# Optimization experiments

Hardware: AMD Instinct MI355X
Metric: run time of the kernel (lower is better)

The kernel has to match this reference:

```python
import jax, jax.numpy as jnp
import numpy as np

LATENT_SHAPES = [(192, 2, 2), (48, 4, 4), (24, 8, 8), (12, 16, 16), (6, 32, 32)]
B = 4          # batch
M = 32         # num_bases
HT, WT = 32, 32  # target spatial size = spatial size of z[-1] = (H/2, W/2)
EPS = 1e-3
CT = sum(s[0] for s in LATENT_SHAPES)  # 282


def _forward_fft(zs):
    # strided zero-insertion upsample of each latent to (HT, WT), concat channels, 2D FFT
    ups = []
    for zi in zs:
        b, c, h, w = zi.shape
        rh, rw = HT // h, WT // w
        u = jnp.zeros((b, c, HT, WT), zi.dtype).at[..., ::rh, ::rw].set(zi)
        ups.append(u)
    z = jnp.concatenate(ups, axis=1)            # (B, CT, HT, WT)
    return jnp.fft.fftn(z, axes=(-2, -1))       # complex64


def _inverse_fft(v_fft):
    # inverse FFT, take real part, split channels per level, strided downsample
    v = jnp.fft.ifftn(v_fft, axes=(-2, -1)).real  # (B, M, CT, HT, WT)
    splits = np.cumsum([s[0] for s in LATENT_SHAPES])[:-1]
    parts = jnp.split(v, splits, axis=-3)
    out = []
    for vi, (c, h, w) in zip(parts, LATENT_SHAPES):
        rh, rw = HT // h, WT // w
        out.append(vi[..., ::rh, ::rw])           # (B, M, c, h, w)
    return out


def _vector_field(zs, L, lam):
    z_fft = _forward_fft(zs)
    La = (L - jnp.swapaxes(L, -1, -2)).astype(jnp.complex64)        # antisymmetric (M, CT, CT)
    lam_a = (lam - jnp.roll(jnp.flip(lam, (1, 2)), (1, 1), axis=(1, 2))) * 1j  # (M, HT, WT) imaginary
    v_fft = jnp.einsum('mcd,bchw->bmdhw', La, z_fft)                 # (B, M, CT, HT, WT) complex
    v_fft = v_fft * lam_a[None, :, None, :, :]
    return _inverse_fft(v_fft)


def _log_prob(ws, zs, L, lam):
    S_ww = sum(jnp.einsum('bchw,bchw->b', wi, wi) for wi in ws)      # (B,)
    v = _vector_field(zs, L, lam)
    S_zz = sum(jnp.einsum('bnchw,bmchw->bnm', vi, vi) for vi in v)   # (B, M, M)
    S_zw = sum(jnp.einsum('bnchw,bchw->bn', vi, wi) for vi, wi in zip(v, ws))  # (B, M)
    var = jnp.maximum(jnp.mean(jnp.diagonal(S_zz, axis1=-2, axis2=-1), -1), 1e-6)
    std = jnp.sqrt(var)
    S_zz = S_zz / var[:, None, None]
    S_zw = S_zw / std[:, None]
    I = jnp.eye(M, dtype=S_zz.dtype)
    Mm = S_zz + EPS * I
    trace = EPS * S_ww + jnp.einsum('bn,bn->b', S_zw, S_zw)
    Lh = jnp.linalg.cholesky(Mm)
    logdet = 2.0 * jnp.sum(jnp.log(jnp.diagonal(Lh, axis1=-2, axis2=-1)), -1)
    return 0.5 * (logdet - trace)


def setup_inputs() -> dict:
    key = jax.random.key(0)
    ks = jax.random.split(key, 12)
    inp = {}
    for i, (c, h, w) in enumerate(LATENT_SHAPES):
        inp[f'z{i}'] = jax.random.normal(ks[i], (B, c, h, w), jnp.float32)
        inp[f'w{i}'] = jax.random.normal(ks[5 + i], (B, c, h, w), jnp.float32)
    inp['L'] = jax.random.normal(ks[10], (M, CT, CT), jnp.float32) * np.float32(1.0 / np.sqrt(CT))
    inp['lam'] = jax.random.normal(ks[11], (M, HT, WT), jnp.float32)
    return inp


def reference(z0, z1, z2, z3, z4, w0, w1, w2, w3, w4, L, lam):
    return _log_prob([w0, w1, w2, w3, w4], [z0, z1, z2, z3, z4], L, lam)
```

## Files before the change

### kernel.cpp

```cpp
#include <hip/hip_runtime.h>
#include <math.h>

#define NB 4
#define NM 32
#define CTOT 282
#define EPSV 1e-3f

__constant__ int g_cL[5]   = {192,48,24,12,6};
__constant__ int g_hL[5]   = {2,4,8,16,32};
__constant__ int g_coff[5] = {0,192,240,264,276};
__constant__ int g_zo[5]   = {0,768,1536,3072,6144};
__constant__ int g_po[4]   = {0,4,20,84};

__constant__ int t_lo[36] = {0,0,0,0,0,0,0,0,0,0,0,0,0,0,0,0,0,0,0,0,0,0,0,0,
                             1,1,1,1,1,1, 2,2,2, 3,3, 4};
__constant__ int t_d0[36] = {0,8,16,24,32,40,48,56,64,72,80,88,96,104,112,120,
                             128,136,144,152,160,168,176,184,
                             192,200,208,216,224,232, 240,248,256, 264,270, 276};
__constant__ int t_nd[36] = {8,8,8,8,8,8,8,8,8,8,8,8,8,8,8,8,8,8,8,8,8,8,8,8,
                             8,8,8,8,8,8, 8,8,8, 6,6, 6};

__constant__ int dft_l[30]  = {0,0,0, 1,1,1, 2,2,2,2,2,2,
                               3,3,3,3,3,3,3,3,3,3,3,3, 4,4,4,4,4,4};
__constant__ int dft_c0[30] = {0,64,128, 0,16,32, 0,4,8,12,16,20,
                               0,1,2,3,4,5,6,7,8,9,10,11, 0,1,2,3,4,5};
__constant__ int dft_nc[30] = {64,64,64, 16,16,16, 4,4,4,4,4,4,
                               1,1,1,1,1,1,1,1,1,1,1,1, 1,1,1,1,1,1};

#define N_LA     (NM*CTOT*CTOT)
#define OFF_LAT  0
#define OFF_ZRE  (OFF_LAT + N_LA)
#define OFF_ZIM  (OFF_ZRE + NB*12288)
#define OFF_WRE  (OFF_ZIM + NB*12288)
#define OFF_WIM  (OFF_WRE + NB*12288)
#define OFF_LAM  (OFF_WIM + NB*12288)
#define OFF_LAMF (OFF_LAM + NM*1024)
#define OFF_UR   (OFF_LAMF + NM*340)
#define OFF_UI   (OFF_UR + NB*NM*6*340)
#define OFF_VRE  (OFF_UI + NB*NM*6*340)
#define OFF_VIM  (OFF_VRE + NB*NM*12288)
#define OFF_SZZ  (OFF_VIM + NB*NM*12288)
#define OFF_SZW  (OFF_SZZ + NB*NM*NM)
#define OFF_SWW  (OFF_SZW + NB*NM)

#define PRE_LAT   (NM*81)
#define PRE_LAMF  (PRE_LAT + NM)
#define PRE_DFT   (PRE_LAMF + 2*NB*30)
#define PRE_SWW   (PRE_DFT + NB)
#define PRE_ZERO  (PRE_SWW + 17)

__global__ void __launch_bounds__(256) k_pre(
    const float* z0,const float* z1,const float* z2,const float* z3,const float* z4,
    const float* w0,const float* w1,const float* w2,const float* w3,const float* w4,
    const float* __restrict__ L, const float* __restrict__ lam, float* __restrict__ ws){
  __shared__ float shm[3136];
  int bid = blockIdx.x, t = threadIdx.x;
  if (bid < PRE_LAT){
    float* A  = shm;
    float* Bt = shm + 1056;
    int m = bid/81; int tl = bid%81;
    int d0 = (tl/9)*32, c0 = (tl%9)*32;
    const float* Lm = L + (size_t)m*CTOT*CTOT;
    for (int i=t;i<1024;i+=256){
      int r=i>>5, c=i&31;
      A[r*33+c]  = (c0+r<CTOT && d0+c<CTOT) ? Lm[(c0+r)*CTOT + d0+c] : 0.f;
      Bt[r*33+c] = (d0+r<CTOT && c0+c<CTOT) ? Lm[(d0+r)*CTOT + c0+c] : 0.f;
    }
    __syncthreads();
    float* out = ws + OFF_LAT + (size_t)m*CTOT*CTOT;
    for (int i=t;i<1024;i+=256){
      int r=i>>5, c=i&31;
      if (d0+r<CTOT && c0+c<CTOT)
        out[(size_t)(d0+r)*CTOT + c0+c] = A[c*33+r] - Bt[r*33+c];
    }
    return;
  }
  if (bid < PRE_LAMF){
    float* sA = shm;
    float* f3 = shm + 1024;
    float* f2 = shm + 1280;
    float* f1 = shm + 1344;
    int m = bid - PRE_LAT;
    for (int k=t;k<1024;k+=256){
      int ky=k>>5, kx=k&31;
      int nk = (((32-ky)&31)<<5) | ((32-kx)&31);
      float v = lam[(m<<10)+k] - lam[(m<<10)+nk];
      sA[k]=v;
      ws[OFF_LAM+(m<<10)+k]=v;
    }
    __syncthreads();
    { int s=t; int ky=s>>4, kx=s&15;
      float v = sA[(ky<<5)+kx]+sA[((ky+16)<<5)+kx]+sA[(ky<<5)+kx+16]+sA[((ky+16)<<5)+kx+16];
      f3[s]=v; ws[OFF_LAMF+m*340+84+s]=v; }
    __syncthreads();
    if (t<64){ int ky=t>>3, kx=t&7;
      float v = f3[(ky<<4)+kx]+f3[((ky+8)<<4)+kx]+f3[(ky<<4)+kx+8]+f3[((ky+8)<<4)+kx+8];
      f2[t]=v; ws[OFF_LAMF+m*340+20+t]=v; }
    __syncthreads();
    if (t<16){ int ky=t>>2, kx=t&3;
      float v = f2[(ky<<3)+kx]+f2[((ky+4)<<3)+kx]+f2[(ky<<3)+kx+4]+f2[((ky+4)<<3)+kx+4];
      f1[t]=v; ws[OFF_LAMF+m*340+4+t]=v; }
    __syncthreads();
    if (t<4){ int ky=t>>1, kx=t&1;
      float v = f1[(ky<<2)+kx]+f1[((ky+2)<<2)+kx]+f1[(ky<<2)+kx+2]+f1[((ky+2)<<2)+kx+2];
      ws[OFF_LAMF+m*340+t]=v; }
    return;
  }
  if (bid < PRE_DFT){
    float* sIn = shm;
    float* s1r = shm + 1024;
    float* s1i = shm + 2048;
    float* lc  = shm + 3072;
    float* lsn = shm + 3104;
    int i0 = bid - PRE_LAMF;
    int which = i0 / (NB*30);
    int rem = i0 % (NB*30);
    int b = rem / 30, j = rem % 30;
    int l = dft_l[j], c0 = dft_c0[j], nc = dft_nc[j];
    int h = g_hL[l], n = h*h;
    int elems = nc*n;
    const float* src;
    switch (which*5 + l){
      case 0: src=z0; break; case 1: src=z1; break; case 2: src=z2; break;
      case 3: src=z3; break; case 4: src=z4; break;
      case 5: src=w0; break; case 6: src=w1; break; case 7: src=w2; break;
      case 8: src=w3; break; default: src=w4; break;
    }
    for (int i=t;i<elems;i+=256) sIn[i] = src[(b*g_cL[l] + c0)*n + i];
    if (t<h){
      float ang = -6.2831853071795864f * (float)t / (float)h;
      lc[t] = cosf(ang); lsn[t] = sinf(ang);
    }
    __syncthreads();
    for (int p=t;p<elems;p+=256){
      int p2=p%n, cc=p/n;
      int y=p2/h, kx=p2-y*h;
      float re=0.f, im=0.f;
      for (int x=0;x<h;x++){
        int id = (kx*x)%h;
        float v = sIn[cc*n + y*h + x];
        re += v*lc[id]; im += v*lsn[id];
      }
      s1r[p]=re; s1i[p]=im;
    }
    __syncthreads();
    float scale = which ? 1.0f/(float)h : 1.0f;
    float* outR = ws + (which?OFF_WRE:OFF_ZRE) + b*12288 + g_zo[l] + c0*n;
    float* outI = ws + (which?OFF_WIM:OFF_ZIM) + b*12288 + g_zo[l] + c0*n;
    for (int p=t;p<elems;p+=256){
      int p2=p%n, cc=p/n;
      int ky=p2/h, kx=p2-(p2/h)*h;
      float re=0.f, im=0.f;
      for (int y=0;y<h;y++){
        int id=(ky*y)%h;
        float c=lc[id], s=lsn[id];
        float ar=s1r[cc*n + y*h + kx], ai=s1i[cc*n + y*h + kx];
        re += ar*c - ai*s;
        im += ar*s + ai*c;
      }
      outR[p]=re*scale; outI[p]=im*scale;
    }
    return;
  }
  if (bid < PRE_SWW){
    float* red = shm;
    int b = bid - PRE_DFT;
    const float* ptr[5] = {w0,w1,w2,w3,w4};
    float s = 0.f;
    for (int l=0;l<5;l++){
      int sz = g_cL[l]*g_hL[l]*g_hL[l];
      const float* p = ptr[l] + b*sz;
      for (int i=t;i<sz;i+=256){ float v=p[i]; s += v*v; }
    }
    red[t]=s; __syncthreads();
    for (int o=128;o>0;o>>=1){ if (t<o) red[t]+=red[t+o]; __syncthreads(); }
    if (t==0) ws[OFF_SWW + b] = red[0];
    return;
  }
  int i = (bid - PRE_SWW)*256 + t;
  if (i < NB*NM*NM + NB*NM) ws[OFF_SZZ + i] = 0.f;
}

__global__ void k_u(float* __restrict__ ws){
  __shared__ float pr[1024], pi[1024], q3r[256],q3i[256],q2r[64],q2i[64],q1r[16],q1i[16];
  int bid = blockIdx.x, t = threadIdx.x;
  int c = bid%6; int m = (bid/6)%NM; int b = bid/(6*NM);
  const float* la = ws+OFF_LAM+(m<<10);
  const float* zr = ws+OFF_ZRE+b*12288+6144+(c<<10);
  const float* zi = ws+OFF_ZIM+b*12288+6144+(c<<10);
  for (int k=t;k<1024;k+=256){ float f=la[k]; pr[k]=f*zr[k]; pi[k]=f*zi[k]; }
  __syncthreads();
  size_t base = (size_t)((b*NM+m)*6+c)*340;
  float* UR = ws+OFF_UR+base; float* UI = ws+OFF_UI+base;
  { int s=t; int ky=s>>4, kx=s&15;
    float r = pr[(ky<<5)+kx]+pr[((ky+16)<<5)+kx]+pr[(ky<<5)+kx+16]+pr[((ky+16)<<5)+kx+16];
    float ii= pi[(ky<<5)+kx]+pi[((ky+16)<<5)+kx]+pi[(ky<<5)+kx+16]+pi[((ky+16)<<5)+kx+16];
    q3r[s]=r; q3i[s]=ii; UR[84+s]=r; UI[84+s]=ii; }
  __syncthreads();
  if (t<64){ int ky=t>>3, kx=t&7;
    float r = q3r[(ky<<4)+kx]+q3r[((ky+8)<<4)+kx]+q3r[(ky<<4)+kx+8]+q3r[((ky+8)<<4)+kx+8];
    float ii= q3i[(ky<<4)+kx]+q3i[((ky+8)<<4)+kx]+q3i[(ky<<4)+kx+8]+q3i[((ky+8)<<4)+kx+8];
    q2r[t]=r; q2i[t]=ii; UR[20+t]=r; UI[20+t]=ii; }
  __syncthreads();
  if (t<16){ int ky=t>>2, kx=t&3;
    float r = q2r[(ky<<3)+kx]+q2r[((ky+4)<<3)+kx]+q2r[(ky<<3)+kx+4]+q2r[((ky+4)<<3)+kx+4];
    float ii= q2i[(ky<<3)+kx]+q2i[((ky+4)<<3)+kx]+q2i[(ky<<3)+kx+4]+q2i[((ky+4)<<3)+kx+4];
    q1r[t]=r; q1i[t]=ii; UR[4+t]=r; UI[4+t]=ii; }
  __syncthreads();
  if (t<4){ int ky=t>>1, kx=t&1;
    float r = q1r[(ky<<2)+kx]+q1r[((ky+2)<<2)+kx]+q1r[(ky<<2)+kx+2]+q1r[((ky+2)<<2)+kx+2];
    float ii= q1i[(ky<<2)+kx]+q1i[((ky+2)<<2)+kx]+q1i[(ky<<2)+kx+2]+q1i[((ky+2)<<2)+kx+2];
    UR[t]=r; UI[t]=ii; }
}

__global__ void __launch_bounds__(256) k_fold(float* __restrict__ ws){
  __shared__ float smem[9444];
  float* pre  = smem;
  float* pim  = smem + 2720;
  float* sLa  = smem + 5440;
  float* c64r = smem + 7712;
  float* c64i = smem + 8224;
  float* c16r = smem + 8736;
  float* c16i = smem + 8864;
  float* c4r  = smem + 8992;
  float* c4i  = smem + 9024;
  float* lamf = smem + 9056;
  float* ssla = smem + 9396;

  int t = threadIdx.x, bid = blockIdx.x;
  int tile = bid % 36;
  int m = (bid/36) % NM;
  int b = bid / (36*NM);
  int lo = t_lo[tile], d0 = t_d0[tile], nd = t_nd[tile];
  int ho = g_hL[lo];
  int nbins = ho*ho;
  const float* zreb = ws + OFF_ZRE + b*12288;
  const float* zimb = ws + OFF_ZIM + b*12288;
  const float* latm = ws + OFF_LAT + (size_t)m*CTOT*CTOT;

  for (int i=t;i<340;i+=256) lamf[i] = ws[OFF_LAMF + m*340 + i];
  for (int i=t;i<nd*282;i+=256){ int d=i/282, c=i-d*282; sLa[d*284+c] = latm[(size_t)(d0+d)*CTOT + c]; }
  if (t<nd*6){ int d=t/6, c=t-d*6; ssla[t] = latm[(size_t)(d0+d)*CTOT + 276 + c]; }

  int lA, kkA, c0A, nA, nred, wrt, offP;
  if (t<64){ lA=0; kkA=t>>4; c0A=(t&15)*12; nA=4; nred=4; wrt=((t&15)==0); offP=0; }
  else if (t<128){ int i=t-64; lA=1; kkA=i>>2; c0A=(i&3)*12; nA=16; nred=2; wrt=((i&3)==0); offP=4; }
  else { int i=t-128; lA=2; kkA=i>>1; c0A=(i&1)*12; nA=64; nred=1; wrt=((i&1)==0); offP=20; }
  float zAr[12], zAi[12], zBr[12], zBi[12];
  {
    const float* zr = zreb + g_zo[lA] + kkA;
    const float* zi = zimb + g_zo[lA] + kkA;
    #pragma unroll
    for (int c=0;c<12;c++){ zAr[c]=zr[(c0A+c)*nA]; zAi[c]=zi[(c0A+c)*nA]; }
    const float* zr3 = zreb + 3072 + t;
    const float* zi3 = zimb + 3072 + t;
    #pragma unroll
    for (int c=0;c<12;c++){ zBr[c]=zr3[c*256]; zBi[c]=zi3[c*256]; }
  }
  __syncthreads();

  int offA = g_coff[lA] + c0A;
  for (int d=0; d<nd; d++){
    const float* la = sLa + d*284;
    float prA=0.f, piA=0.f, prB=0.f, piB=0.f;
    #pragma unroll
    for (int c=0;c<12;c++){ float a=la[offA+c]; prA+=a*zAr[c]; piA+=a*zAi[c]; }
    #pragma unroll
    for (int c=0;c<12;c++){ float a=la[264+c]; prB+=a*zBr[c]; piB+=a*zBi[c]; }
    if (nred==4){
      prA += __shfl_xor(prA,1); piA += __shfl_xor(piA,1);
      prA += __shfl_xor(prA,2); piA += __shfl_xor(piA,2);
      prA += __shfl_xor(prA,4); piA += __shfl_xor(piA,4);
      prA += __shfl_xor(prA,8); piA += __shfl_xor(piA,8);
    } else if (nred==2){
      prA += __shfl_xor(prA,1); piA += __shfl_xor(piA,1);
      prA += __shfl_xor(prA,2); piA += __shfl_xor(piA,2);
    } else {
      prA += __shfl_xor(prA,1); piA += __shfl_xor(piA,1);
    }
    if (wrt){ pre[d*340 + offP + kkA] = prA; pim[d*340 + offP + kkA] = piA; }
    pre[d*340+84+t] = prB; pim[d*340+84+t] = piB;
  }
  __syncthreads();

  float sc = (float)ho/1024.f;
  if (lo==4){
    const float* lamA = ws + OFF_LAM + (m<<10);
    float* vRb = ws + OFF_VRE + (size_t)(b*NM+m)*12288 + 6144;
    float* vIb = ws + OFF_VIM + (size_t)(b*NM+m)*12288 + 6144;
    const float* z4r = zreb + 6144;
    const float* z4i = zimb + 6144;
    for (int q=t; q<1024; q+=256){
      int ky=q>>5, kx=q&31;
      int a0=((ky&1)<<1)|(kx&1);
      int a1=4+(((ky&3)<<2)|(kx&3));
      int a2=20+(((ky&7)<<3)|(kx&7));
      int a3=84+(((ky&15)<<4)|(kx&15));
      float zr_[6], zi_[6];
      #pragma unroll
      for (int c=0;c<6;c++){ zr_[c]=z4r[(c<<10)+q]; zi_[c]=z4i[(c<<10)+q]; }
      float lm = lamA[q]*sc;
      for (int d=0; d<6; d++){
        const float* pd = pre + d*340; const float* qd = pim + d*340;
        float Br = pd[a0]+pd[a1]+pd[a2]+pd[a3];
        float Bi = qd[a0]+qd[a1]+qd[a2]+qd[a3];
        #pragma unroll
        for (int c=0;c<6;c++){ float a=ssla[d*6+c]; Br+=a*zr_[c]; Bi+=a*zi_[c]; }
        vRb[(d<<10)+q] = -lm*Bi;
        vIb[(d<<10)+q] =  lm*Br;
      }
    }
    return;
  }

  if (lo<3){
    for (int idx=t; idx<nd*64; idx+=256){
      int d=idx>>6, k2=idx&63, ky=k2>>3, kx=k2&7;
      const float* pd = pre + d*340 + 84; const float* qd = pim + d*340 + 84;
      float r=0.f, ii=0.f;
      #pragma unroll
      for (int jy=0;jy<2;jy++)
        #pragma unroll
        for (int jx=0;jx<2;jx++){
          int a = ((ky+8*jy)<<4) | (kx+8*jx);
          float f = lamf[84+a];
          r += f*pd[a]; ii += f*qd[a];
        }
      if (lo<2){ float f=lamf[20+k2]; r+=f*pre[d*340+20+k2]; ii+=f*pim[d*340+20+k2]; }
      c64r[idx]=r; c64i[idx]=ii;
    }
  }
  __syncthreads();
  if (lo<2){
    for (int idx=t; idx<nd*16; idx+=256){
      int d=idx>>4, k2=idx&15, ky=k2>>2, kx=k2&3, base=d<<6;
      float r = c64r[base+(ky<<3)+kx]+c64r[base+((ky+4)<<3)+kx]+c64r[base+(ky<<3)+kx+4]+c64r[base+((ky+4)<<3)+kx+4];
      float ii= c64i[base+(ky<<3)+kx]+c64i[base+((ky+4)<<3)+kx]+c64i[base+(ky<<3)+kx+4]+c64i[base+((ky+4)<<3)+kx+4];
      if (lo<1){ float f=lamf[4+k2]; r+=f*pre[d*340+4+k2]; ii+=f*pim[d*340+4+k2]; }
      c16r[idx]=r; c16i[idx]=ii;
    }
  }
  __syncthreads();
  if (lo==0 && t<nd*4){
    int d=t>>2, k2=t&3, ky=k2>>1, kx=k2&1, base=d<<4;
    c4r[t]=c16r[base+(ky<<2)+kx]+c16r[base+((ky+2)<<2)+kx]+c16r[base+(ky<<2)+kx+2]+c16r[base+((ky+2)<<2)+kx+2];
    c4i[t]=c16i[base+(ky<<2)+kx]+c16i[base+((ky+2)<<2)+kx]+c16i[base+(ky<<2)+kx+2]+c16i[base+((ky+2)<<2)+kx+2];
  }
  __syncthreads();

  int dlb = d0 - g_coff[lo];
  float* vRb = ws + OFF_VRE + (size_t)(b*NM+m)*12288 + g_zo[lo];
  float* vIb = ws + OFF_VIM + (size_t)(b*NM+m)*12288 + g_zo[lo];
  const float* URg = ws + OFF_UR + (size_t)((b*NM+m)*6)*340 + g_po[lo];
  const float* UIg = ws + OFF_UI + (size_t)((b*NM+m)*6)*340 + g_po[lo];
  for (int idx=t; idx<nd*nbins; idx+=256){
    int d=idx/nbins, bin=idx-d*nbins;
    int ky=bin/ho, kx=bin-ky*ho;
    const float* pd = pre + d*340; const float* qd = pim + d*340;
    float Br = pd[((ky&1)<<1)|(kx&1)], Bi = qd[((ky&1)<<1)|(kx&1)];
    if (lo>=1){ int ix=4+(((ky&3)<<2)|(kx&3)); Br+=pd[ix]; Bi+=qd[ix]; }
    if (lo>=2){ int ix=20+(((ky&7)<<3)|(kx&7)); Br+=pd[ix]; Bi+=qd[ix]; }
    if (lo>=3){ int ix=84+(((ky&15)<<4)|(kx&15)); Br+=pd[ix]; Bi+=qd[ix]; }
    float lf = lamf[g_po[lo]+bin];
    float Vr = lf*Br, Vi = lf*Bi;
    if (lo==2){ Vr+=c64r[(d<<6)+bin]; Vi+=c64i[(d<<6)+bin]; }
    else if (lo==1){ Vr+=c16r[(d<<4)+bin]; Vi+=c16i[(d<<4)+bin]; }
    else if (lo==0){ Vr+=c4r[(d<<2)+bin]; Vi+=c4i[(d<<2)+bin]; }
    #pragma unroll
    for (int c=0;c<6;c++){ float a=ssla[d*6+c]; Vr+=a*URg[c*340+bin]; Vi+=a*UIg[c*340+bin]; }
    int ob = (dlb+d)*nbins + bin;
    vRb[ob] = -sc*Vi;
    vIb[ob] =  sc*Vr;
  }
}

__global__ void __launch_bounds__(256) k_gram(float* __restrict__ ws){
  __shared__ float tile[32*260];
  __shared__ float wv[256];
  int t = threadIdx.x;
  int bid = blockIdx.x;
  int b = bid / 96, ch = bid % 96;
  int half = ch / 48;
  int k0 = (ch % 48) * 256;
  const float* V = ws + (half?OFF_VIM:OFF_VRE);
  const float* W = ws + (half?OFF_WIM:OFF_WRE) + b*12288 + k0;
  for (int i=t;i<32*256;i+=256){
    int r=i>>8, c=i&255;
    tile[r*260+c] = V[(size_t)(b*NM+r)*12288 + k0 + c];
  }
  wv[t] = W[t];
  __syncthreads();
  const float4* tf = (const float4*)tile;
  int n0 = t>>5, mm = t&31;
  float acc0=0.f, acc1=0.f, acc2=0.f, acc3=0.f;
  const float4* rm = tf + mm*65;
  const float4* r0 = tf + n0*65;
  const float4* r1 = tf + (n0+8)*65;
  const float4* r2 = tf + (n0+16)*65;
  const float4* r3 = tf + (n0+24)*65;
  for (int k4=0;k4<64;k4++){
    float4 vm = rm[k4];
    float4 v0 = r0[k4];
    float4 v1 = r1[k4];
    float4 v2 = r2[k4];
    float4 v3 = r3[k4];
    acc0 += v0.x*vm.x + v0.y*vm.y + v0.z*vm.z + v0.w*vm.w;
    acc1 += v1.x*vm.x + v1.y*vm.y + v1.z*vm.z + v1.w*vm.w;
    acc2 += v2.x*vm.x + v2.y*vm.y + v2.z*vm.z + v2.w*vm.w;
    acc3 += v3.x*vm.x + v3.y*vm.y + v3.z*vm.z + v3.w*vm.w;
  }
  float* szz = ws + OFF_SZZ + (b<<10);
  atomicAdd(&szz[(n0<<5) + mm], acc0);
  atomicAdd(&szz[((n0+8)<<5) + mm], acc1);
  atomicAdd(&szz[((n0+16)<<5) + mm], acc2);
  atomicAdd(&szz[((n0+24)<<5) + mm], acc3);
  if (t < 32){
    const float4* rn = tf + t*65;
    const float4* wf = (const float4*)wv;
    float acc=0.f;
    for (int k4=0;k4<64;k4++){
      float4 a = rn[k4]; float4 wq = wf[k4];
      acc += a.x*wq.x + a.y*wq.y + a.z*wq.z + a.w*wq.w;
    }
    atomicAdd(&ws[OFF_SZW + (b<<5) + t], acc);
  }
}

__global__ void k_final(float* __restrict__ ws, float* __restrict__ out){
  __shared__ float A[32][33];
  __shared__ float svar;
  int b = blockIdx.x, t = threadIdx.x;
  const float* szz = ws + OFF_SZZ + (b<<10);
  if (t==0){
    float s=0.f;
    for (int i=0;i<32;i++) s += szz[i*33];
    svar = fmaxf(s/32.0f, 1e-6f);
  }
  __syncthreads();
  float var = svar;
  for (int i=t;i<1024;i+=64){
    int r=i>>5, c=i&31;
    A[r][c] = szz[i]/var + ((r==c)?EPSV:0.0f);
  }
  __syncthreads();
  for (int j=0;j<32;j++){
    if (t==0) A[j][j] = sqrtf(A[j][j]);
    __syncthreads();
    if (t>j && t<32) A[t][j] /= A[j][j];
    __syncthreads();
    if (t>j && t<32){
      float lij = A[t][j];
      for (int k=j+1;k<=t;k++) A[t][k] -= lij*A[k][j];
    }
    __syncthreads();
  }
  if (t==0){
    float logdet=0.f;
    for (int j=0;j<32;j++) logdet += logf(A[j][j]);
    logdet *= 2.0f;
    const float* szw = ws + OFF_SZW + (b<<5);
    float s2=0.f;
    for (int n=0;n<32;n++) s2 += szw[n]*szw[n];
    float trace = EPSV*ws[OFF_SWW + b] + s2/var;
    out[b] = 0.5f*(logdet - trace);
  }
}

extern "C" void kernel_launch(void* const* d_in, const int* in_sizes, int n_in,
                              void* d_out, int out_size, void* d_ws, size_t ws_size,
                              hipStream_t stream){
  const float* z0 = (const float*)d_in[0];
  const float* w0 = (const float*)d_in[1];
  const float* z1 = (const float*)d_in[2];
  const float* w1 = (const float*)d_in[3];
  const float* z2 = (const float*)d_in[4];
  const float* w2 = (const float*)d_in[5];
  const float* z3 = (const float*)d_in[6];
  const float* w3 = (const float*)d_in[7];
  const float* z4 = (const float*)d_in[8];
  const float* w4 = (const float*)d_in[9];
  const float* L   = (const float*)d_in[10];
  const float* lam = (const float*)d_in[11];
  float* ws = (float*)d_ws;
  float* out = (float*)d_out;

  k_pre<<<PRE_ZERO, 256, 0, stream>>>(z0,z1,z2,z3,z4,w0,w1,w2,w3,w4, L, lam, ws);
  k_u<<<NB*NM*6, 256, 0, stream>>>(ws);
  k_fold<<<NB*NM*36, 256, 0, stream>>>(ws);
  k_gram<<<NB*96, 256, 0, stream>>>(ws);
  k_final<<<NB, 64, 0, stream>>>(ws, out);
}
```

Before: 219.4 us.

## Rebalance k_fold tiles, replace shuffle reductions with shared partials, stage U in LDS

The k_fold kernel now runs 48 tiles of 6 (or 3) channels instead of 36 tiles of 8, and orders blocks so that batches sharing an m sit next to each other. This gives more blocks and better balance, and should improve L2 reuse of each m's L slice. The cross-lane shuffle reductions are replaced by per-thread partial sums written to shared memory, which a second pass then reduces. The La coefficients are read as float4, and the U arrays are staged into LDS before the final loop instead of being read from global memory on every use. The cost is an extra sync and reduction pass, plus aliasing of sLa with the c64 buffers in shared memory.

```diff
diff --git a/kernel.cpp b/kernel.cpp
--- a/kernel.cpp
+++ b/kernel.cpp
@@ -12,13 +12,15 @@
 __constant__ int g_zo[5]   = {0,768,1536,3072,6144};
 __constant__ int g_po[4]   = {0,4,20,84};
 
-__constant__ int t_lo[36] = {0,0,0,0,0,0,0,0,0,0,0,0,0,0,0,0,0,0,0,0,0,0,0,0,
-                             1,1,1,1,1,1, 2,2,2, 3,3, 4};
-__constant__ int t_d0[36] = {0,8,16,24,32,40,48,56,64,72,80,88,96,104,112,120,
-                             128,136,144,152,160,168,176,184,
-                             192,200,208,216,224,232, 240,248,256, 264,270, 276};
-__constant__ int t_nd[36] = {8,8,8,8,8,8,8,8,8,8,8,8,8,8,8,8,8,8,8,8,8,8,8,8,
-                             8,8,8,8,8,8, 8,8,8, 6,6, 6};
+__constant__ int t_lo[48] = {0,0,0,0,0,0,0,0,0,0,0,0,0,0,0,0,
+                             0,0,0,0,0,0,0,0,0,0,0,0,0,0,0,0,
+                             1,1,1,1,1,1,1,1, 2,2,2,2, 3,3, 4,4};
+__constant__ int t_d0[48] = {0,6,12,18,24,30,36,42,48,54,60,66,72,78,84,90,
+                             96,102,108,114,120,126,132,138,144,150,156,162,168,174,180,186,
+                             192,198,204,210,216,222,228,234, 240,246,252,258, 264,270, 276,279};
+__constant__ int t_nd[48] = {6,6,6,6,6,6,6,6,6,6,6,6,6,6,6,6,
+                             6,6,6,6,6,6,6,6,6,6,6,6,6,6,6,6,
+                             6,6,6,6,6,6,6,6, 6,6,6,6, 6,6, 3,3};
 
 __constant__ int dft_l[30]  = {0,0,0, 1,1,1, 2,2,2,2,2,2,
                                3,3,3,3,3,3,3,3,3,3,3,3, 4,4,4,4,4,4};
@@ -214,23 +216,26 @@
 }
 
 __global__ void __launch_bounds__(256) k_fold(float* __restrict__ ws){
-  __shared__ float smem[9444];
-  float* pre  = smem;
-  float* pim  = smem + 2720;
-  float* sLa  = smem + 5440;
-  float* c64r = smem + 7712;
-  float* c64i = smem + 8224;
-  float* c16r = smem + 8736;
-  float* c16i = smem + 8864;
-  float* c4r  = smem + 8992;
-  float* c4i  = smem + 9024;
-  float* lamf = smem + 9056;
-  float* ssla = smem + 9396;
+  __shared__ float smem[9232];
+  float* pre   = smem;
+  float* pim   = smem + 2040;
+  float* partr = smem + 4080;
+  float* parti = smem + 5616;
+  float* sLa   = smem + 7152;
+  float* c64r  = smem + 7152;
+  float* c64i  = smem + 7536;
+  float* c16r  = smem + 7920;
+  float* c16i  = smem + 8016;
+  float* c4r   = smem + 8112;
+  float* c4i   = smem + 8136;
+  float* lamf  = smem + 8856;
+  float* ssla  = smem + 9196;
 
   int t = threadIdx.x, bid = blockIdx.x;
-  int tile = bid % 36;
-  int m = (bid/36) % NM;
-  int b = bid / (36*NM);
+  int m    = bid / (NB*48);
+  int rem  = bid % (NB*48);
+  int b    = rem / 48;
+  int tile = rem % 48;
   int lo = t_lo[tile], d0 = t_d0[tile], nd = t_nd[tile];
   int ho = g_hL[lo];
   int nbins = ho*ho;
@@ -242,10 +247,10 @@
   for (int i=t;i<nd*282;i+=256){ int d=i/282, c=i-d*282; sLa[d*284+c] = latm[(size_t)(d0+d)*CTOT + c]; }
   if (t<nd*6){ int d=t/6, c=t-d*6; ssla[t] = latm[(size_t)(d0+d)*CTOT + 276 + c]; }
 
-  int lA, kkA, c0A, nA, nred, wrt, offP;
-  if (t<64){ lA=0; kkA=t>>4; c0A=(t&15)*12; nA=4; nred=4; wrt=((t&15)==0); offP=0; }
-  else if (t<128){ int i=t-64; lA=1; kkA=i>>2; c0A=(i&3)*12; nA=16; nred=2; wrt=((i&3)==0); offP=4; }
-  else { int i=t-128; lA=2; kkA=i>>1; c0A=(i&1)*12; nA=64; nred=1; wrt=((i&1)==0); offP=20; }
+  int lA, kkA, c0A, nA;
+  if (t<64){ lA=0; kkA=t&3; c0A=(t>>2)*12; nA=4; }
+  else if (t<128){ int i=t-64; lA=1; kkA=i&15; c0A=(i>>4)*12; nA=16; }
+  else { int i=t-128; lA=2; kkA=i&63; c0A=(i>>6)*12; nA=64; }
   float zAr[12], zAi[12], zBr[12], zBi[12];
   {
     const float* zr = zreb + g_zo[lA] + kkA;
@@ -261,33 +266,39 @@
 
   int offA = g_coff[lA] + c0A;
   for (int d=0; d<nd; d++){
-    const float* la = sLa + d*284;
+    const float4* laA = (const float4*)(sLa + d*284 + offA);
+    const float4* laB = (const float4*)(sLa + d*284 + 264);
+    float4 a0=laA[0], a1=laA[1], a2=laA[2];
+    float4 b0=laB[0], b1=laB[1], b2=laB[2];
+    float av[12] = {a0.x,a0.y,a0.z,a0.w, a1.x,a1.y,a1.z,a1.w, a2.x,a2.y,a2.z,a2.w};
+    float bv[12] = {b0.x,b0.y,b0.z,b0.w, b1.x,b1.y,b1.z,b1.w, b2.x,b2.y,b2.z,b2.w};
     float prA=0.f, piA=0.f, prB=0.f, piB=0.f;
     #pragma unroll
-    for (int c=0;c<12;c++){ float a=la[offA+c]; prA+=a*zAr[c]; piA+=a*zAi[c]; }
+    for (int c=0;c<12;c++){ prA+=av[c]*zAr[c]; piA+=av[c]*zAi[c]; }
     #pragma unroll
-    for (int c=0;c<12;c++){ float a=la[264+c]; prB+=a*zBr[c]; piB+=a*zBi[c]; }
-    if (nred==4){
-      prA += __shfl_xor(prA,1); piA += __shfl_xor(piA,1);
-      prA += __shfl_xor(prA,2); piA += __shfl_xor(piA,2);
-      prA += __shfl_xor(prA,4); piA += __shfl_xor(piA,4);
-      prA += __shfl_xor(prA,8); piA += __shfl_xor(piA,8);
-    } else if (nred==2){
-      prA += __shfl_xor(prA,1); piA += __shfl_xor(piA,1);
-      prA += __shfl_xor(prA,2); piA += __shfl_xor(piA,2);
-    } else {
-      prA += __shfl_xor(prA,1); piA += __shfl_xor(piA,1);
-    }
-    if (wrt){ pre[d*340 + offP + kkA] = prA; pim[d*340 + offP + kkA] = piA; }
-    pre[d*340+84+t] = prB; pim[d*340+84+t] = piB;
+    for (int c=0;c<12;c++){ prB+=bv[c]*zBr[c]; piB+=bv[c]*zBi[c]; }
+    partr[(d<<8)+t]=prA; parti[(d<<8)+t]=piA;
+    pre[d*340+84+t]=prB; pim[d*340+84+t]=piB;
+  }
+  __syncthreads();
+
+  for (int idx=t; idx<nd*84; idx+=256){
+    int d=idx/84, s=idx-d*84;
+    int base=d<<8;
+    float r=0.f, ii=0.f;
+    if (s<4){ for (int ch=0;ch<16;ch++){ int p=base+((ch<<2)|s); r+=partr[p]; ii+=parti[p]; } }
+    else if (s<20){ int kk=s-4; for (int ch=0;ch<4;ch++){ int p=base+64+((ch<<4)|kk); r+=partr[p]; ii+=parti[p]; } }
+    else { int kk=s-20; for (int ch=0;ch<2;ch++){ int p=base+128+((ch<<6)|kk); r+=partr[p]; ii+=parti[p]; } }
+    pre[d*340+s]=r; pim[d*340+s]=ii;
   }
   __syncthreads();
 
   float sc = (float)ho/1024.f;
   if (lo==4){
+    int dlb = d0 - 276;
     const float* lamA = ws + OFF_LAM + (m<<10);
-    float* vRb = ws + OFF_VRE + (size_t)(b*NM+m)*12288 + 6144;
-    float* vIb = ws + OFF_VIM + (size_t)(b*NM+m)*12288 + 6144;
+    float* vRb = ws + OFF_VRE + (size_t)(b*NM+m)*12288 + 6144 + (dlb<<10);
+    float* vIb = ws + OFF_VIM + (size_t)(b*NM+m)*12288 + 6144 + (dlb<<10);
     const float* z4r = zreb + 6144;
     const float* z4i = zimb + 6144;
     for (int q=t; q<1024; q+=256){
@@ -300,7 +311,7 @@
       #pragma unroll
       for (int c=0;c<6;c++){ zr_[c]=z4r[(c<<10)+q]; zi_[c]=z4i[(c<<10)+q]; }
       float lm = lamA[q]*sc;
-      for (int d=0; d<6; d++){
+      for (int d=0; d<nd; d++){
         const float* pd = pre + d*340; const float* qd = pim + d*340;
         float Br = pd[a0]+pd[a1]+pd[a2]+pd[a3];
         float Bi = qd[a0]+qd[a1]+qd[a2]+qd[a3];
@@ -330,6 +341,15 @@
       c64r[idx]=r; c64i[idx]=ii;
     }
   }
+  {
+    const float* URg = ws + OFF_UR + (size_t)((b*NM+m)*6)*340 + g_po[lo];
+    const float* UIg = ws + OFF_UI + (size_t)((b*NM+m)*6)*340 + g_po[lo];
+    for (int idx=t; idx<6*nbins; idx+=256){
+      int c=idx/nbins, bin=idx-c*nbins;
+      partr[idx]=URg[c*340+bin];
+      parti[idx]=UIg[c*340+bin];
+    }
+  }
   __syncthreads();
   if (lo<2){
     for (int idx=t; idx<nd*16; idx+=256){
@@ -351,8 +371,6 @@
   int dlb = d0 - g_coff[lo];
   float* vRb = ws + OFF_VRE + (size_t)(b*NM+m)*12288 + g_zo[lo];
   float* vIb = ws + OFF_VIM + (size_t)(b*NM+m)*12288 + g_zo[lo];
-  const float* URg = ws + OFF_UR + (size_t)((b*NM+m)*6)*340 + g_po[lo];
-  const float* UIg = ws + OFF_UI + (size_t)((b*NM+m)*6)*340 + g_po[lo];
   for (int idx=t; idx<nd*nbins; idx+=256){
     int d=idx/nbins, bin=idx-d*nbins;
     int ky=bin/ho, kx=bin-ky*ho;
@@ -367,7 +385,7 @@
     else if (lo==1){ Vr+=c16r[(d<<4)+bin]; Vi+=c16i[(d<<4)+bin]; }
     else if (lo==0){ Vr+=c4r[(d<<2)+bin]; Vi+=c4i[(d<<2)+bin]; }
     #pragma unroll
-    for (int c=0;c<6;c++){ float a=ssla[d*6+c]; Vr+=a*URg[c*340+bin]; Vi+=a*UIg[c*340+bin]; }
+    for (int c=0;c<6;c++){ float a=ssla[d*6+c]; Vr+=a*partr[c*nbins+bin]; Vi+=a*parti[c*nbins+bin]; }
     int ob = (dlb+d)*nbins + bin;
     vRb[ob] = -sc*Vi;
     vIb[ob] =  sc*Vr;
@@ -486,7 +504,7 @@
 
   k_pre<<<PRE_ZERO, 256, 0, stream>>>(z0,z1,z2,z3,z4,w0,w1,w2,w3,w4, L, lam, ws);
   k_u<<<NB*NM*6, 256, 0, stream>>>(ws);
-  k_fold<<<NB*NM*36, 256, 0, stream>>>(ws);
+  k_fold<<<NB*NM*48, 256, 0, stream>>>(ws);
   k_gram<<<NB*96, 256, 0, stream>>>(ws);
   k_final<<<NB, 64, 0, stream>>>(ws, out);
 }
```

Result: faster. 213.3 us (-2.8%).
